# Performance work log

Hardware: AMD Instinct MI355X
Metric: run time of the kernel (lower is better)

## Reference

```python
import jax, jax.numpy as jnp
import numpy as np

B, H, W, C = 16, 128, 128, 192
WS, SHIFT, HEADS = 8, 4, 6
N = WS * WS
HD = C // HEADS
SCALE = HD ** -0.5
EPS = 1e-5


def _rel_pos_index():
    coords = np.stack(np.meshgrid(np.arange(WS), np.arange(WS), indexing='ij')).reshape(2, -1)
    rel = (coords[:, :, None] - coords[:, None, :]).transpose(1, 2, 0)
    rel[..., 0] += WS - 1
    rel[..., 1] += WS - 1
    rel[..., 0] *= 2 * WS - 1
    return rel.sum(-1)  # [N, N] int


def _attn_mask():
    img = np.zeros((H, W), np.float32)
    sl = [(0, H - WS), (H - WS, H - SHIFT), (H - SHIFT, H)]
    cnt = 0
    for h0, h1 in sl:
        for w0, w1 in sl:
            img[h0:h1, w0:w1] = cnt
            cnt += 1
    mw = img.reshape(H // WS, WS, W // WS, WS).transpose(0, 2, 1, 3).reshape(-1, N)
    am = mw[:, None, :] - mw[:, :, None]
    return np.where(am != 0, np.float32(-100.0), np.float32(0.0))  # [nW, N, N]


REL_IDX = jnp.asarray(_rel_pos_index())
ATTN_MASK = jnp.asarray(_attn_mask())


def _ln(x, g, b):
    mu = x.mean(-1, keepdims=True)
    var = ((x - mu) ** 2).mean(-1, keepdims=True)
    return (x - mu) * jax.lax.rsqrt(var + EPS) * g + b


def setup_inputs() -> dict:
    key = jax.random.key(0)
    ks = jax.random.split(key, 12)
    d = {
        'x': jax.random.normal(ks[0], (B, H * W, C), jnp.float32),
        'norm1_g': jnp.ones((C,), jnp.float32),
        'norm1_b': jnp.zeros((C,), jnp.float32),
        'qkv_w': jax.random.normal(ks[1], (3 * C, C), jnp.float32) * 0.02,
        'qkv_b': jnp.zeros((3 * C,), jnp.float32),
        'proj_w': jax.random.normal(ks[2], (C, C), jnp.float32) * 0.02,
        'proj_b': jnp.zeros((C,), jnp.float32),
        'rpb_table': jax.random.normal(ks[3], ((2 * WS - 1) ** 2, HEADS), jnp.float32) * 0.02,
        'norm2_g': jnp.ones((C,), jnp.float32),
        'norm2_b': jnp.zeros((C,), jnp.float32),
        'fc1_w': jax.random.normal(ks[4], (4 * C, C), jnp.float32) * 0.02,
        'fc1_b': jnp.zeros((4 * C,), jnp.float32),
        'fc2_w': jax.random.normal(ks[5], (C, 4 * C), jnp.float32) * 0.02,
        'fc2_b': jnp.zeros((C,), jnp.float32),
    }
    return d


def reference(x, norm1_g, norm1_b, qkv_w, qkv_b, proj_w, proj_b, rpb_table,
              norm2_g, norm2_b, fc1_w, fc1_b, fc2_w, fc2_b):
    shortcut = x
    h = _ln(x, norm1_g, norm1_b).reshape(B, H, W, C)
    # cyclic shift (SW-MSA)
    h = jnp.roll(h, shift=(-SHIFT, -SHIFT), axis=(1, 2))
    # window partition -> [B*nW, N, C]
    h = h.reshape(B, H // WS, WS, W // WS, WS, C).transpose(0, 1, 3, 2, 4, 5)
    xw = h.reshape(-1, N, C)
    Bw = xw.shape[0]
    nW = (H // WS) * (W // WS)
    # qkv projection
    qkv = xw @ qkv_w.T + qkv_b  # [Bw, N, 3C]
    qkv = qkv.reshape(Bw, N, 3, HEADS, HD).transpose(2, 0, 3, 1, 4)
    q, k, v = qkv[0], qkv[1], qkv[2]  # [Bw, HEADS, N, HD]
    attn = jnp.einsum('bhnd,bhmd->bhnm', q * SCALE, k)
    # relative position bias gather: [N*N, HEADS] -> [HEADS, N, N]
    bias = rpb_table[REL_IDX.reshape(-1)].reshape(N, N, HEADS).transpose(2, 0, 1)
    attn = attn + bias[None]
    # shift mask add per-window
    attn = attn.reshape(B, nW, HEADS, N, N) + ATTN_MASK[None, :, None, :, :]
    attn = jax.nn.softmax(attn.reshape(Bw, HEADS, N, N), axis=-1)
    out = jnp.einsum('bhnm,bhmd->bhnd', attn, v)
    out = out.transpose(0, 2, 1, 3).reshape(Bw, N, C)
    out = out @ proj_w.T + proj_b
    # window reverse
    out = out.reshape(B, H // WS, W // WS, WS, WS, C).transpose(0, 1, 3, 2, 4, 5)
    out = out.reshape(B, H, W, C)
    out = jnp.roll(out, shift=(SHIFT, SHIFT), axis=(1, 2)).reshape(B, H * W, C)
    h = shortcut + out
    # MLP with residual
    m = _ln(h, norm2_g, norm2_b)
    m = jax.nn.gelu(m @ fc1_w.T + fc1_b, approximate=False)
    m = m @ fc2_w.T + fc2_b
    return h + m
```

## Files before the change

### kernel.cpp

```cpp
#include <hip/hip_runtime.h>
#include <hip/hip_bf16.h>

typedef __bf16 bf16;
typedef __bf16 bf16x8 __attribute__((ext_vector_type(8)));
typedef float f32x4 __attribute__((ext_vector_type(4)));

#define MFMA16(a, b, c) __builtin_amdgcn_mfma_f32_16x16x32_bf16(a, b, c, 0, 0, 0)

#define SCALE_Q 0.17677669529663687f

__global__ __launch_bounds__(256) void prep_kernel(
    const float* __restrict__ qkv_w, const float* __restrict__ proj_w,
    const float* __restrict__ fc1_w, const float* __restrict__ fc2_w,
    const float* __restrict__ rpb,
    bf16* __restrict__ wqkv, bf16* __restrict__ wproj,
    bf16* __restrict__ wfc1, bf16* __restrict__ wfc2,
    float* __restrict__ bias_full) {
  const int i = blockIdx.x * 256 + threadIdx.x;
  if (i < 110592) wqkv[i] = (bf16)qkv_w[i];
  if (i < 36864)  wproj[i] = (bf16)proj_w[i];
  if (i < 147456) { wfc1[i] = (bf16)fc1_w[i]; wfc2[i] = (bf16)fc2_w[i]; }
  if (i < 24576) {
    const int head = i >> 12;
    const int row = (i >> 6) & 63, col = i & 63;
    const int idx = ((row >> 3) - (col >> 3) + 7) * 15 + ((row & 7) - (col & 7) + 7);
    bias_full[i] = rpb[idx * 6 + head];
  }
}

__device__ __forceinline__ int region8(int tok, int wy, int wx) {
  const int gh = wy * 8 + (tok >> 3), gw = wx * 8 + (tok & 7);
  const int rs = (gh < 120) ? 0 : ((gh < 124) ? 1 : 2);
  const int cs = (gw < 120) ? 0 : ((gw < 124) ? 1 : 2);
  return rs * 3 + cs;
}

__global__ __launch_bounds__(384, 1) void swin_block_kernel(
    const float* __restrict__ x,
    const float* __restrict__ n1g, const float* __restrict__ n1b,
    const bf16* __restrict__ wqkv, const float* __restrict__ qkv_b,
    const bf16* __restrict__ wproj, const float* __restrict__ proj_b,
    const float* __restrict__ bias_full,
    const float* __restrict__ n2g, const float* __restrict__ n2b,
    const bf16* __restrict__ wfc1, const float* __restrict__ fc1_b,
    const bf16* __restrict__ wfc2, const float* __restrict__ fc2_b,
    float* __restrict__ out) {
  __shared__ __align__(16) char smem[129024];
  bf16*  q_s  = (bf16*)(smem);
  bf16*  k_s  = (bf16*)(smem + 24576);
  bf16*  vT_s = (bf16*)(smem + 49152);
  bf16*  a_s  = (bf16*)(smem + 73728);
  bf16*  p_s  = (bf16*)(smem + 73728);
  bf16*  ao_s = (bf16*)(smem + 73728);
  float* h_s  = (float*)(smem);
  bf16*  m_s  = (bf16*)(smem + 73728);
  bf16*  g_s  = (bf16*)(smem + 99328);

  const int lane = threadIdx.x & 63, waveid = threadIdx.x >> 6;
  const int c = lane & 15, quad = lane >> 4;
  const int window = blockIdx.x;
  const int bi = window >> 8, w_in = window & 255;
  const int wy = w_in >> 4, wx = w_in & 15;
  const f32x4 fzero = {0.f, 0.f, 0.f, 0.f};

  for (int it = 0; it < 11; it++) {
    const int n = waveid * 11 + it;
    if (n < 64) {
      const int oh = (wy * 8 + (n >> 3) + 4) & 127;
      const int ow = (wx * 8 + (n & 7) + 4) & 127;
      const float* xr = x + (size_t)(bi * 16384 + oh * 128 + ow) * 192;
      float v0 = xr[lane], v1 = xr[lane + 64], v2 = xr[lane + 128];
      float s = v0 + v1 + v2;
      float s2 = v0 * v0 + v1 * v1 + v2 * v2;
#pragma unroll
      for (int off = 1; off < 64; off <<= 1) {
        s += __shfl_xor(s, off);
        s2 += __shfl_xor(s2, off);
      }
      const float mu = s * (1.f / 192.f);
      const float rinv = rsqrtf(s2 * (1.f / 192.f) - mu * mu + 1e-5f);
      a_s[n * 200 + lane]       = (bf16)((v0 - mu) * rinv * n1g[lane]       + n1b[lane]);
      a_s[n * 200 + lane + 64]  = (bf16)((v1 - mu) * rinv * n1g[lane + 64]  + n1b[lane + 64]);
      a_s[n * 200 + lane + 128] = (bf16)((v2 - mu) * rinv * n1g[lane + 128] + n1b[lane + 128]);
    }
  }
  __syncthreads();

  {
    f32x4 acc[4][6];
#pragma unroll
    for (int i = 0; i < 4; i++)
#pragma unroll
      for (int j = 0; j < 6; j++) acc[i][j] = fzero;
#pragma unroll
    for (int ks = 0; ks < 6; ks++) {
      bf16x8 a[4], w[6];
#pragma unroll
      for (int i = 0; i < 4; i++)
        a[i] = *(const bf16x8*)&a_s[(16 * i + c) * 200 + ks * 32 + quad * 8];
#pragma unroll
      for (int j = 0; j < 6; j++)
        w[j] = *(const bf16x8*)(wqkv +
            (size_t)(waveid * 96 + 16 * j + c) * 192 + ks * 32 + quad * 8);
#pragma unroll
      for (int i = 0; i < 4; i++)
#pragma unroll
        for (int j = 0; j < 6; j++) acc[i][j] = MFMA16(a[i], w[j], acc[i][j]);
    }
    const int which = waveid >> 1;
#pragma unroll
    for (int j = 0; j < 6; j++) {
      const int col = waveid * 96 + 16 * j + c;
      const int sub = col - which * 192;
      const int head = sub >> 5, d = sub & 31;
      const float bias = qkv_b[col];
#pragma unroll
      for (int i = 0; i < 4; i++)
#pragma unroll
        for (int r = 0; r < 4; r++) {
          const int n = 16 * i + 4 * quad + r;
          const float val = acc[i][j][r] + bias;
          if (which == 0)      q_s[head * 2048 + n * 32 + d] = (bf16)(val * SCALE_Q);
          else if (which == 1) k_s[head * 2048 + n * 32 + d] = (bf16)val;
          else                 vT_s[head * 2048 + d * 64 + n] = (bf16)val;
        }
    }
  }
  __syncthreads();

  f32x4 o[4][2];
  {
    const int head = waveid;
    bf16x8 aq[4], bk[4];
#pragma unroll
    for (int i = 0; i < 4; i++)
      aq[i] = *(const bf16x8*)&q_s[head * 2048 + (16 * i + c) * 32 + quad * 8];
#pragma unroll
    for (int j = 0; j < 4; j++)
      bk[j] = *(const bf16x8*)&k_s[head * 2048 + (16 * j + c) * 32 + quad * 8];
    f32x4 s[4][4];
#pragma unroll
    for (int i = 0; i < 4; i++)
#pragma unroll
      for (int j = 0; j < 4; j++) s[i][j] = fzero;
#pragma unroll
    for (int i = 0; i < 4; i++)
#pragma unroll
      for (int j = 0; j < 4; j++) s[i][j] = MFMA16(aq[i], bk[j], s[i][j]);

    const float* bfp = bias_full + head * 4096;
#pragma unroll
    for (int i = 0; i < 4; i++)
#pragma unroll
      for (int r = 0; r < 4; r++) {
        const int row = 16 * i + 4 * quad + r;
#pragma unroll
        for (int j = 0; j < 4; j++) s[i][j][r] += bfp[row * 64 + 16 * j + c];
      }

    if (wy == 15 || wx == 15) {
      int creg[4];
#pragma unroll
      for (int j = 0; j < 4; j++) creg[j] = region8(16 * j + c, wy, wx);
#pragma unroll
      for (int i = 0; i < 4; i++)
#pragma unroll
        for (int r = 0; r < 4; r++) {
          const int rreg = region8(16 * i + 4 * quad + r, wy, wx);
#pragma unroll
          for (int j = 0; j < 4; j++)
            if (rreg != creg[j]) s[i][j][r] -= 100.f;
        }
    }

#pragma unroll
    for (int i = 0; i < 4; i++)
#pragma unroll
      for (int r = 0; r < 4; r++) {
        float mx = fmaxf(fmaxf(s[i][0][r], s[i][1][r]), fmaxf(s[i][2][r], s[i][3][r]));
#pragma unroll
        for (int off = 1; off < 16; off <<= 1) mx = fmaxf(mx, __shfl_xor(mx, off));
        float sum = 0.f;
#pragma unroll
        for (int j = 0; j < 4; j++) {
          const float p = __expf(s[i][j][r] - mx);
          s[i][j][r] = p;
          sum += p;
        }
#pragma unroll
        for (int off = 1; off < 16; off <<= 1) sum += __shfl_xor(sum, off);
        const float inv = 1.f / sum;
        const int row = 16 * i + 4 * quad + r;
#pragma unroll
        for (int j = 0; j < 4; j++)
          p_s[head * 4608 + row * 72 + 16 * j + c] = (bf16)(s[i][j][r] * inv);
      }

#pragma unroll
    for (int i = 0; i < 4; i++)
#pragma unroll
      for (int tn = 0; tn < 2; tn++) o[i][tn] = fzero;
#pragma unroll
    for (int ks = 0; ks < 2; ks++) {
      bf16x8 ap[4], bv[2];
#pragma unroll
      for (int i = 0; i < 4; i++)
        ap[i] = *(const bf16x8*)&p_s[head * 4608 + (16 * i + c) * 72 + ks * 32 + quad * 8];
#pragma unroll
      for (int tn = 0; tn < 2; tn++)
        bv[tn] = *(const bf16x8*)&vT_s[head * 2048 + (16 * tn + c) * 64 + ks * 32 + quad * 8];
#pragma unroll
      for (int i = 0; i < 4; i++)
#pragma unroll
        for (int tn = 0; tn < 2; tn++) o[i][tn] = MFMA16(ap[i], bv[tn], o[i][tn]);
    }
  }
  __syncthreads();

#pragma unroll
  for (int i = 0; i < 4; i++)
#pragma unroll
    for (int tn = 0; tn < 2; tn++)
#pragma unroll
      for (int r = 0; r < 4; r++)
        ao_s[(16 * i + 4 * quad + r) * 200 + waveid * 32 + 16 * tn + c] = (bf16)o[i][tn][r];
  __syncthreads();

  {
    f32x4 acc[4][2];
#pragma unroll
    for (int i = 0; i < 4; i++)
#pragma unroll
      for (int j = 0; j < 2; j++) acc[i][j] = fzero;
#pragma unroll
    for (int ks = 0; ks < 6; ks++) {
      bf16x8 a[4], w[2];
#pragma unroll
      for (int i = 0; i < 4; i++)
        a[i] = *(const bf16x8*)&ao_s[(16 * i + c) * 200 + ks * 32 + quad * 8];
#pragma unroll
      for (int j = 0; j < 2; j++)
        w[j] = *(const bf16x8*)(wproj +
            (size_t)(waveid * 32 + 16 * j + c) * 192 + ks * 32 + quad * 8);
#pragma unroll
      for (int i = 0; i < 4; i++)
#pragma unroll
        for (int j = 0; j < 2; j++) acc[i][j] = MFMA16(a[i], w[j], acc[i][j]);
    }
#pragma unroll
    for (int i = 0; i < 4; i++)
#pragma unroll
      for (int r = 0; r < 4; r++) {
        const int n = 16 * i + 4 * quad + r;
        const int oh = (wy * 8 + (n >> 3) + 4) & 127;
        const int ow = (wx * 8 + (n & 7) + 4) & 127;
        const float* xr = x + (size_t)(bi * 16384 + oh * 128 + ow) * 192;
#pragma unroll
        for (int j = 0; j < 2; j++) {
          const int col = waveid * 32 + 16 * j + c;
          h_s[n * 192 + col] = acc[i][j][r] + proj_b[col] + xr[col];
        }
      }
  }
  __syncthreads();

  for (int it = 0; it < 11; it++) {
    const int n = waveid * 11 + it;
    if (n < 64) {
      float v0 = h_s[n * 192 + lane], v1 = h_s[n * 192 + lane + 64],
            v2 = h_s[n * 192 + lane + 128];
      float s = v0 + v1 + v2;
      float s2 = v0 * v0 + v1 * v1 + v2 * v2;
#pragma unroll
      for (int off = 1; off < 64; off <<= 1) {
        s += __shfl_xor(s, off);
        s2 += __shfl_xor(s2, off);
      }
      const float mu = s * (1.f / 192.f);
      const float rinv = rsqrtf(s2 * (1.f / 192.f) - mu * mu + 1e-5f);
      m_s[n * 200 + lane]       = (bf16)((v0 - mu) * rinv * n2g[lane]       + n2b[lane]);
      m_s[n * 200 + lane + 64]  = (bf16)((v1 - mu) * rinv * n2g[lane + 64]  + n2b[lane + 64]);
      m_s[n * 200 + lane + 128] = (bf16)((v2 - mu) * rinv * n2g[lane + 128] + n2b[lane + 128]);
    }
  }
  __syncthreads();

  f32x4 oacc[4][2];
#pragma unroll
  for (int i = 0; i < 4; i++)
#pragma unroll
    for (int j = 0; j < 2; j++) oacc[i][j] = fzero;

  for (int chunk = 0; chunk < 4; chunk++) {
    f32x4 gacc[4][2];
#pragma unroll
    for (int i = 0; i < 4; i++)
#pragma unroll
      for (int j = 0; j < 2; j++) gacc[i][j] = fzero;
#pragma unroll
    for (int ks = 0; ks < 6; ks++) {
      bf16x8 a[4], w[2];
#pragma unroll
      for (int i = 0; i < 4; i++)
        a[i] = *(const bf16x8*)&m_s[(16 * i + c) * 200 + ks * 32 + quad * 8];
#pragma unroll
      for (int j = 0; j < 2; j++)
        w[j] = *(const bf16x8*)(wfc1 +
            (size_t)(chunk * 192 + waveid * 32 + 16 * j + c) * 192 + ks * 32 + quad * 8);
#pragma unroll
      for (int i = 0; i < 4; i++)
#pragma unroll
        for (int j = 0; j < 2; j++) gacc[i][j] = MFMA16(a[i], w[j], gacc[i][j]);
    }
#pragma unroll
    for (int i = 0; i < 4; i++)
#pragma unroll
      for (int j = 0; j < 2; j++) {
        const int lcol = waveid * 32 + 16 * j + c;
        const float fb = fc1_b[chunk * 192 + lcol];
#pragma unroll
        for (int r = 0; r < 4; r++) {
          float val = gacc[i][j][r] + fb;
          val = 0.5f * val * (1.f + erff(val * 0.70710678118654752f));
          g_s[(16 * i + 4 * quad + r) * 200 + lcol] = (bf16)val;
        }
      }
    __syncthreads();
#pragma unroll
    for (int ks = 0; ks < 6; ks++) {
      bf16x8 a[4], w[2];
#pragma unroll
      for (int i = 0; i < 4; i++)
        a[i] = *(const bf16x8*)&g_s[(16 * i + c) * 200 + ks * 32 + quad * 8];
#pragma unroll
      for (int j = 0; j < 2; j++)
        w[j] = *(const bf16x8*)(wfc2 +
            (size_t)(waveid * 32 + 16 * j + c) * 768 + chunk * 192 + ks * 32 + quad * 8);
#pragma unroll
      for (int i = 0; i < 4; i++)
#pragma unroll
        for (int j = 0; j < 2; j++) oacc[i][j] = MFMA16(a[i], w[j], oacc[i][j]);
    }
    __syncthreads();
  }

#pragma unroll
  for (int i = 0; i < 4; i++)
#pragma unroll
    for (int r = 0; r < 4; r++) {
      const int n = 16 * i + 4 * quad + r;
      const int oh = (wy * 8 + (n >> 3) + 4) & 127;
      const int ow = (wx * 8 + (n & 7) + 4) & 127;
      float* orow = out + (size_t)(bi * 16384 + oh * 128 + ow) * 192;
#pragma unroll
      for (int j = 0; j < 2; j++) {
        const int col = waveid * 32 + 16 * j + c;
        orow[col] = oacc[i][j][r] + fc2_b[col] + h_s[n * 192 + col];
      }
    }
}

extern "C" void kernel_launch(void* const* d_in, const int* in_sizes, int n_in,
                              void* d_out, int out_size, void* d_ws, size_t ws_size,
                              hipStream_t stream) {
  const float* x      = (const float*)d_in[0];
  const float* n1g    = (const float*)d_in[1];
  const float* n1b    = (const float*)d_in[2];
  const float* qkv_w  = (const float*)d_in[3];
  const float* qkv_b  = (const float*)d_in[4];
  const float* proj_w = (const float*)d_in[5];
  const float* proj_b = (const float*)d_in[6];
  const float* rpb    = (const float*)d_in[7];
  const float* n2g    = (const float*)d_in[8];
  const float* n2b    = (const float*)d_in[9];
  const float* fc1_w  = (const float*)d_in[10];
  const float* fc1_b  = (const float*)d_in[11];
  const float* fc2_w  = (const float*)d_in[12];
  const float* fc2_b  = (const float*)d_in[13];

  char* ws = (char*)d_ws;
  float* biasf = (float*)(ws);
  bf16*  wqkv  = (bf16*)(ws + 98304);
  bf16*  wproj = (bf16*)(ws + 98304 + 221184);
  bf16*  wfc1  = (bf16*)(ws + 98304 + 221184 + 73728);
  bf16*  wfc2  = (bf16*)(ws + 98304 + 221184 + 73728 + 294912);

  prep_kernel<<<576, 256, 0, stream>>>(qkv_w, proj_w, fc1_w, fc2_w, rpb,
                                       wqkv, wproj, wfc1, wfc2, biasf);
  swin_block_kernel<<<4096, 384, 0, stream>>>(
      x, n1g, n1b, wqkv, qkv_b, wproj, proj_b, biasf,
      n2g, n2b, wfc1, fc1_b, wfc2, fc2_b, (float*)d_out);
}
```

Measured before the change: 1.308 ms.

## Shrink LDS footprint to allow multiple blocks per CU via buffer aliasing

Reworks shared memory layout so buffers alias more aggressively (LN1 output over q, swizzled P buffer over q/k region, small reduction buffer), cutting LDS from about 126KB to about 79KB and raising launch bounds to allow more resident blocks per CU. The residual h is kept in registers instead of shared memory, and LN2 is computed from MFMA-layout registers with a cross-wave reduction through a small shared buffer. Extra barriers are added to protect the aliased regions, and register pressure grows with the hreg array, which could cause spills under the tighter occupancy bound.

```diff
diff --git a/kernel.cpp b/kernel.cpp
--- a/kernel.cpp
+++ b/kernel.cpp
@@ -35,7 +35,7 @@
   return rs * 3 + cs;
 }
 
-__global__ __launch_bounds__(384, 1) void swin_block_kernel(
+__global__ __launch_bounds__(384, 3) void swin_block_kernel(
     const float* __restrict__ x,
     const float* __restrict__ n1g, const float* __restrict__ n1b,
     const bf16* __restrict__ wqkv, const float* __restrict__ qkv_b,
@@ -45,16 +45,15 @@
     const bf16* __restrict__ wfc1, const float* __restrict__ fc1_b,
     const bf16* __restrict__ wfc2, const float* __restrict__ fc2_b,
     float* __restrict__ out) {
-  __shared__ __align__(16) char smem[129024];
+  __shared__ __align__(16) char smem[80896];
+  bf16*  a_s  = (bf16*)(smem);
   bf16*  q_s  = (bf16*)(smem);
   bf16*  k_s  = (bf16*)(smem + 24576);
   bf16*  vT_s = (bf16*)(smem + 49152);
-  bf16*  a_s  = (bf16*)(smem + 73728);
-  bf16*  p_s  = (bf16*)(smem + 73728);
-  bf16*  ao_s = (bf16*)(smem + 73728);
-  float* h_s  = (float*)(smem);
-  bf16*  m_s  = (bf16*)(smem + 73728);
-  bf16*  g_s  = (bf16*)(smem + 99328);
+  bf16*  ao_s = (bf16*)(smem);
+  float* red_s = (float*)(smem + 25600);
+  bf16*  m_s  = (bf16*)(smem + 29696);
+  bf16*  g_s  = (bf16*)(smem + 55296);
 
   const int lane = threadIdx.x & 63, waveid = threadIdx.x >> 6;
   const int c = lane & 15, quad = lane >> 4;
@@ -62,6 +61,12 @@
   const int bi = window >> 8, w_in = window & 255;
   const int wy = w_in >> 4, wx = w_in & 15;
   const f32x4 fzero = {0.f, 0.f, 0.f, 0.f};
+
+  auto p_ptr = [&](int head, int row, int colbyte) -> bf16* {
+    int off = (row << 7) + colbyte;
+    off ^= (row & 7) << 4;
+    return (bf16*)(smem + (head << 13) + off);
+  };
 
   for (int it = 0; it < 11; it++) {
     const int n = waveid * 11 + it;
@@ -107,6 +112,7 @@
 #pragma unroll
         for (int j = 0; j < 6; j++) acc[i][j] = MFMA16(a[i], w[j], acc[i][j]);
     }
+    __syncthreads();
     const int which = waveid >> 1;
 #pragma unroll
     for (int j = 0; j < 6; j++) {
@@ -138,6 +144,8 @@
 #pragma unroll
     for (int j = 0; j < 4; j++)
       bk[j] = *(const bf16x8*)&k_s[head * 2048 + (16 * j + c) * 32 + quad * 8];
+    __syncthreads();
+
     f32x4 s[4][4];
 #pragma unroll
     for (int i = 0; i < 4; i++)
@@ -193,7 +201,7 @@
         const int row = 16 * i + 4 * quad + r;
 #pragma unroll
         for (int j = 0; j < 4; j++)
-          p_s[head * 4608 + row * 72 + 16 * j + c] = (bf16)(s[i][j][r] * inv);
+          *p_ptr(head, row, (16 * j + c) * 2) = (bf16)(s[i][j][r] * inv);
       }
 
 #pragma unroll
@@ -205,7 +213,7 @@
       bf16x8 ap[4], bv[2];
 #pragma unroll
       for (int i = 0; i < 4; i++)
-        ap[i] = *(const bf16x8*)&p_s[head * 4608 + (16 * i + c) * 72 + ks * 32 + quad * 8];
+        ap[i] = *(const bf16x8*)p_ptr(head, 16 * i + c, ks * 64 + quad * 16);
 #pragma unroll
       for (int tn = 0; tn < 2; tn++)
         bv[tn] = *(const bf16x8*)&vT_s[head * 2048 + (16 * tn + c) * 64 + ks * 32 + quad * 8];
@@ -226,6 +234,7 @@
         ao_s[(16 * i + 4 * quad + r) * 200 + waveid * 32 + 16 * tn + c] = (bf16)o[i][tn][r];
   __syncthreads();
 
+  float hreg[4][2][4];
   {
     f32x4 acc[4][2];
 #pragma unroll
@@ -258,30 +267,49 @@
 #pragma unroll
         for (int j = 0; j < 2; j++) {
           const int col = waveid * 32 + 16 * j + c;
-          h_s[n * 192 + col] = acc[i][j][r] + proj_b[col] + xr[col];
+          hreg[i][j][r] = acc[i][j][r] + proj_b[col] + xr[col];
         }
       }
   }
-  __syncthreads();
-
-  for (int it = 0; it < 11; it++) {
-    const int n = waveid * 11 + it;
-    if (n < 64) {
-      float v0 = h_s[n * 192 + lane], v1 = h_s[n * 192 + lane + 64],
-            v2 = h_s[n * 192 + lane + 128];
-      float s = v0 + v1 + v2;
-      float s2 = v0 * v0 + v1 * v1 + v2 * v2;
-#pragma unroll
-      for (int off = 1; off < 64; off <<= 1) {
-        s += __shfl_xor(s, off);
+
+#pragma unroll
+  for (int i = 0; i < 4; i++)
+#pragma unroll
+    for (int r = 0; r < 4; r++) {
+      float s1 = hreg[i][0][r] + hreg[i][1][r];
+      float s2 = hreg[i][0][r] * hreg[i][0][r] + hreg[i][1][r] * hreg[i][1][r];
+#pragma unroll
+      for (int off = 1; off < 16; off <<= 1) {
+        s1 += __shfl_xor(s1, off);
         s2 += __shfl_xor(s2, off);
       }
-      const float mu = s * (1.f / 192.f);
-      const float rinv = rsqrtf(s2 * (1.f / 192.f) - mu * mu + 1e-5f);
-      m_s[n * 200 + lane]       = (bf16)((v0 - mu) * rinv * n2g[lane]       + n2b[lane]);
-      m_s[n * 200 + lane + 64]  = (bf16)((v1 - mu) * rinv * n2g[lane + 64]  + n2b[lane + 64]);
-      m_s[n * 200 + lane + 128] = (bf16)((v2 - mu) * rinv * n2g[lane + 128] + n2b[lane + 128]);
-    }
+      if (c == 0) {
+        const int n = 16 * i + 4 * quad + r;
+        red_s[n * 16 + waveid] = s1;
+        red_s[n * 16 + 8 + waveid] = s2;
+      }
+    }
+  __syncthreads();
+  {
+    const int col0 = waveid * 32 + c, col1 = col0 + 16;
+    const float g0 = n2g[col0], b0 = n2b[col0];
+    const float g1 = n2g[col1], b1 = n2b[col1];
+#pragma unroll
+    for (int i = 0; i < 4; i++)
+#pragma unroll
+      for (int r = 0; r < 4; r++) {
+        const int n = 16 * i + 4 * quad + r;
+        const f32x4 lo = *(const f32x4*)&red_s[n * 16 + 0];
+        const f32x4 hi = *(const f32x4*)&red_s[n * 16 + 4];
+        const f32x4 qlo = *(const f32x4*)&red_s[n * 16 + 8];
+        const f32x4 qhi = *(const f32x4*)&red_s[n * 16 + 12];
+        const float s1 = lo[0] + lo[1] + lo[2] + lo[3] + hi[0] + hi[1];
+        const float s2 = qlo[0] + qlo[1] + qlo[2] + qlo[3] + qhi[0] + qhi[1];
+        const float mu = s1 * (1.f / 192.f);
+        const float rinv = rsqrtf(s2 * (1.f / 192.f) - mu * mu + 1e-5f);
+        m_s[n * 200 + col0] = (bf16)((hreg[i][0][r] - mu) * rinv * g0 + b0);
+        m_s[n * 200 + col1] = (bf16)((hreg[i][1][r] - mu) * rinv * g1 + b1);
+      }
   }
   __syncthreads();
 
@@ -355,7 +383,7 @@
 #pragma unroll
       for (int j = 0; j < 2; j++) {
         const int col = waveid * 32 + 16 * j + c;
-        orow[col] = oacc[i][j][r] + fc2_b[col] + h_s[n * 192 + col];
+        orow[col] = oacc[i][j][r] + fc2_b[col] + hreg[i][j][r];
       }
     }
 }
```

Result: slower. 1.419 ms (+8.5%).
